# Kernel optimization log

Measured on AMD Instinct MI355X. Metric: run time of the kernel, lower is better.

The kernel has to match this reference:

```python
import jax, jax.numpy as jnp
import numpy as np
from functools import partial

VS, VT, E, H = 32000, 32000, 512, 1024
B, S, T = 32, 64, 64


def gru_cell(x, h, Wih, Whh, bih, bhh):
    # PyTorch GRU gate order: r, z, n
    gi = x @ Wih.T + bih
    gh = h @ Whh.T + bhh
    ir, iz, inn = jnp.split(gi, 3, axis=-1)
    hr, hz, hn = jnp.split(gh, 3, axis=-1)
    r = jax.nn.sigmoid(ir + hr)
    z = jax.nn.sigmoid(iz + hz)
    n = jnp.tanh(inn + r * hn)
    return (1.0 - z) * n + z * h


def setup_inputs() -> dict:
    key = jax.random.key(0)
    ks = jax.random.split(key, 20)
    s = 0.02
    src = jax.random.randint(ks[0], (B, S), 0, VS)
    tgt = jax.random.randint(ks[1], (B, T), 0, VT)
    src_embed = (jax.random.normal(ks[2], (VS, E)) * s).at[0].set(0.0)  # padding_idx=0
    tgt_embed = (jax.random.normal(ks[3], (VT, E)) * s).at[0].set(0.0)
    enc_Wih = jax.random.normal(ks[4], (3 * H, E)) * s
    enc_Whh = jax.random.normal(ks[5], (3 * H, H)) * s
    enc_bih = jax.random.normal(ks[6], (3 * H,)) * s
    enc_bhh = jax.random.normal(ks[7], (3 * H,)) * s
    dec_Wih = jax.random.normal(ks[8], (3 * H, E + H)) * s
    dec_Whh = jax.random.normal(ks[9], (3 * H, H)) * s
    dec_bih = jax.random.normal(ks[10], (3 * H,)) * s
    dec_bhh = jax.random.normal(ks[11], (3 * H,)) * s
    attn_W = jax.random.normal(ks[12], (E, 2 * H)) * s
    attn_b = jax.random.normal(ks[13], (E,)) * s
    v_w = jax.random.normal(ks[14], (E,)) * s
    fc_W = jax.random.normal(ks[15], (VT, H)) * s
    fc_b = jax.random.normal(ks[16], (VT,)) * s
    return dict(src=src, tgt=tgt, src_embed=src_embed, tgt_embed=tgt_embed,
                enc_Wih=enc_Wih, enc_Whh=enc_Whh, enc_bih=enc_bih, enc_bhh=enc_bhh,
                dec_Wih=dec_Wih, dec_Whh=dec_Whh, dec_bih=dec_bih, dec_bhh=dec_bhh,
                attn_W=attn_W, attn_b=attn_b, v_w=v_w, fc_W=fc_W, fc_b=fc_b)


def reference(src, tgt, src_embed, tgt_embed, enc_Wih, enc_Whh, enc_bih, enc_bhh,
              dec_Wih, dec_Whh, dec_bih, dec_bhh, attn_W, attn_b, v_w, fc_W, fc_b):
    # --- encoder: GRU over src ---
    src_emb = src_embed[src]                      # [B,S,E]
    h0 = jnp.zeros((src.shape[0], H), src_emb.dtype)

    def enc_step(h, x):
        h2 = gru_cell(x, h, enc_Wih, enc_Whh, enc_bih, enc_bhh)
        return h2, h2

    h_last, enc_seq = jax.lax.scan(enc_step, h0, jnp.swapaxes(src_emb, 0, 1))
    enc = jnp.swapaxes(enc_seq, 0, 1)             # [B,S,H] encoder_outputs

    # attn linear splits: cat([hidden, enc]) @ attn_W.T == h@Wh.T + enc@We.T
    Wh, We = attn_W[:, :H], attn_W[:, H:]
    enc_proj = jnp.einsum('bsh,eh->bse', enc, We) + attn_b  # [B,S,E]

    # --- decoder with teacher forcing ratio = 1.0 (deterministic) ---
    def dec_step(h, tok):
        emb = tgt_embed[tok]                              # [B,E]
        energy = jnp.tanh(enc_proj + (h @ Wh.T)[:, None, :])  # [B,S,E]
        scores = jnp.einsum('bse,e->bs', energy, v_w)
        w = jax.nn.softmax(scores, axis=1)                # [B,S]
        ctx = jnp.einsum('bs,bsh->bh', w, enc)            # [B,H]
        x = jnp.concatenate([emb, ctx], axis=-1)          # [B,E+H]
        h2 = gru_cell(x, h, dec_Wih, dec_Whh, dec_bih, dec_bhh)
        logits = h2 @ fc_W.T + fc_b                       # [B,VT]
        return h2, logits

    _, logits = jax.lax.scan(dec_step, h_last, tgt[:, :-1].T)  # [T-1,B,VT]
    return jnp.swapaxes(logits, 0, 1)                     # [B,T-1,VT]
```

## Files before the change

### kernel.cpp

```cpp
#include <hip/hip_runtime.h>
#include <hip/hip_bf16.h>

typedef __hip_bfloat16 bf16;
typedef __attribute__((ext_vector_type(8))) __bf16 bf16x8;
typedef __attribute__((ext_vector_type(4))) float f32x4;

#define DEVI __device__ __forceinline__

DEVI float sigm(float x) { return 1.f / (1.f + __expf(-x)); }
DEVI float tanh_fast(float x) { float e = __expf(2.f * x); return 1.f - 2.f / (e + 1.f); }
DEVI float us2f(unsigned short u) { return __uint_as_float(((unsigned)u) << 16); }

DEVI __bf16 f2b(float f) {
    unsigned u = __float_as_uint(f);
    u = u + 0x7FFFu + ((u >> 16) & 1u);
    unsigned short s = (unsigned short)(u >> 16);
    __bf16 b;
    __builtin_memcpy(&b, &s, 2);
    return b;
}

DEVI f32x4 MFMA(bf16x8 a, bf16x8 b, f32x4 c) {
    return __builtin_amdgcn_mfma_f32_16x16x32_bf16(a, b, c, 0, 0, 0);
}

DEVI bf16x8 load8(const bf16* p) { return *reinterpret_cast<const bf16x8*>(p); }
DEVI bf16x8 load8(const float* p) {
    float4 a = *reinterpret_cast<const float4*>(p);
    float4 b = *reinterpret_cast<const float4*>(p + 4);
    bf16x8 r;
    r[0] = f2b(a.x); r[1] = f2b(a.y); r[2] = f2b(a.z); r[3] = f2b(a.w);
    r[4] = f2b(b.x); r[5] = f2b(b.y); r[6] = f2b(b.z); r[7] = f2b(b.w);
    return r;
}

template<typename AT, typename BT, bool GATHER, bool SWAP>
__global__ __launch_bounds__(256)
void gemm_bt(const AT* __restrict__ A, const int* __restrict__ Aidx, int lda,
             const BT* __restrict__ B, int ldb, int boff,
             const float* __restrict__ bias,
             float* __restrict__ C, long ldc,
             int M_real, int K)
{
    __shared__ __attribute__((aligned(16))) bf16 As[128 * 32];
    __shared__ __attribute__((aligned(16))) bf16 Bs[128 * 32];
    const int tid = threadIdx.x;
    const int lane = tid & 63;
    const int w = tid >> 6;
    const int wr = w >> 1, wc = w & 1;
    const int bm = (SWAP ? blockIdx.x : blockIdx.y) * 128;
    const int bn = (SWAP ? blockIdx.y : blockIdx.x) * 128;

    const int l16_0 = (2 * w + 0) * 64 + lane;
    const int l16_1 = (2 * w + 1) * 64 + lane;
    const int row0 = l16_0 >> 2, c0 = l16_0 & 3;
    const int row1 = l16_1 >> 2, c1 = l16_1 & 3;

    long arow0 = GATHER ? (long)Aidx[bm + row0] : (long)(bm + row0);
    long arow1 = GATHER ? (long)Aidx[bm + row1] : (long)(bm + row1);
    const AT* agp0 = A + arow0 * lda + c0 * 8;
    const AT* agp1 = A + arow1 * lda + c1 * 8;
    const BT* bgp0 = B + (long)(bn + row0) * ldb + boff + c0 * 8;
    const BT* bgp1 = B + (long)(bn + row1) * ldb + boff + c1 * 8;

    f32x4 acc[4][4];
    #pragma unroll
    for (int i = 0; i < 4; i++)
        #pragma unroll
        for (int j = 0; j < 4; j++) acc[i][j] = f32x4{0.f, 0.f, 0.f, 0.f};

    const bf16x8* Asv = reinterpret_cast<const bf16x8*>(As);
    const bf16x8* Bsv = reinterpret_cast<const bf16x8*>(Bs);
    bf16x8* AsW = reinterpret_cast<bf16x8*>(As);
    bf16x8* BsW = reinterpret_cast<bf16x8*>(Bs);
    const int kq = lane >> 4;
    const int lrow = lane & 15;

    bf16x8 ra0 = load8(agp0);
    bf16x8 ra1 = load8(agp1);
    bf16x8 rb0 = load8(bgp0);
    bf16x8 rb1 = load8(bgp1);

    for (int k0 = 0; k0 < K; k0 += 32) {
        __syncthreads();
        AsW[l16_0] = ra0; AsW[l16_1] = ra1;
        BsW[l16_0] = rb0; BsW[l16_1] = rb1;
        __syncthreads();

        const int kn = k0 + 32;
        if (kn < K) {
            ra0 = load8(agp0 + kn);
            ra1 = load8(agp1 + kn);
            rb0 = load8(bgp0 + kn);
            rb1 = load8(bgp1 + kn);
        }

        bf16x8 af[4], bfr[4];
        #pragma unroll
        for (int mt = 0; mt < 4; mt++) af[mt] = Asv[(wr * 64 + mt * 16 + lrow) * 4 + kq];
        #pragma unroll
        for (int nt = 0; nt < 4; nt++) bfr[nt] = Bsv[(wc * 64 + nt * 16 + lrow) * 4 + kq];
        #pragma unroll
        for (int mt = 0; mt < 4; mt++)
            #pragma unroll
            for (int nt = 0; nt < 4; nt++)
                acc[mt][nt] = MFMA(af[mt], bfr[nt], acc[mt][nt]);
    }

    const int rbase = kq * 4;
    #pragma unroll
    for (int nt = 0; nt < 4; nt++) {
        const int col = bn + wc * 64 + nt * 16 + lrow;
        const float bv = bias[col];
        #pragma unroll
        for (int mt = 0; mt < 4; mt++) {
            const int rw = bm + wr * 64 + mt * 16 + rbase;
            #pragma unroll
            for (int r = 0; r < 4; r++) {
                const int row = rw + r;
                if (row < M_real) C[(long)row * ldc + col] = acc[mt][nt][r] + bv;
            }
        }
    }
}

__global__ __launch_bounds__(256)
void cvt_f32_bf16(const float* __restrict__ in, bf16* __restrict__ out, int n)
{
    int i = (blockIdx.x * blockDim.x + threadIdx.x) * 4;
    if (i < n) {
        float4 v = *reinterpret_cast<const float4*>(in + i);
        ushort4 o;
        __bf16 b0 = f2b(v.x), b1 = f2b(v.y), b2 = f2b(v.z), b3 = f2b(v.w);
        __builtin_memcpy(&o.x, &b0, 2); __builtin_memcpy(&o.y, &b1, 2);
        __builtin_memcpy(&o.z, &b2, 2); __builtin_memcpy(&o.w, &b3, 2);
        *reinterpret_cast<ushort4*>(out + i) = o;
    }
}

__global__ __launch_bounds__(512)
void enc_step(const bf16* __restrict__ h_bf, const float* __restrict__ h_f,
              const float* __restrict__ X, int t,
              const bf16* __restrict__ Whh, const float* __restrict__ bhh,
              float* __restrict__ h_f_n, bf16* __restrict__ h_bf_n,
              bf16* __restrict__ enc_out,
              const float* __restrict__ attnW, float* __restrict__ pa, int do_pa)
{
    __shared__ float part[8][3][32][16];
    __shared__ float h2s[32][16];
    const int tid = threadIdx.x;
    const int lane = tid & 63;
    const int kw = tid >> 6;
    const int j0 = blockIdx.x * 16;
    const int lrow = lane & 15;
    const int kq = lane >> 4;

    f32x4 acc[3][2];
    #pragma unroll
    for (int g = 0; g < 3; g++) { acc[g][0] = f32x4{0,0,0,0}; acc[g][1] = f32x4{0,0,0,0}; }

    const bf16x8* hv = reinterpret_cast<const bf16x8*>(h_bf);
    const bf16x8* wv = reinterpret_cast<const bf16x8*>(Whh);
    const int kb = kw * 16 + kq;
    const int a0r = lrow * 128 + kb;
    const int a1r = (16 + lrow) * 128 + kb;
    const int b0r = (j0 + lrow) * 128 + kb;
    const int b1r = (1024 + j0 + lrow) * 128 + kb;
    const int b2r = (2048 + j0 + lrow) * 128 + kb;

    #pragma unroll
    for (int kk = 0; kk < 4; kk++) {
        const int o = kk * 4;
        bf16x8 a0 = hv[a0r + o];
        bf16x8 a1 = hv[a1r + o];
        bf16x8 b0 = wv[b0r + o];
        bf16x8 b1 = wv[b1r + o];
        bf16x8 b2 = wv[b2r + o];
        acc[0][0] = MFMA(a0, b0, acc[0][0]); acc[0][1] = MFMA(a1, b0, acc[0][1]);
        acc[1][0] = MFMA(a0, b1, acc[1][0]); acc[1][1] = MFMA(a1, b1, acc[1][1]);
        acc[2][0] = MFMA(a0, b2, acc[2][0]); acc[2][1] = MFMA(a1, b2, acc[2][1]);
    }

    #pragma unroll
    for (int g = 0; g < 3; g++)
        #pragma unroll
        for (int mt = 0; mt < 2; mt++)
            #pragma unroll
            for (int r = 0; r < 4; r++)
                part[kw][g][mt * 16 + kq * 4 + r][lrow] = acc[g][mt][r];
    __syncthreads();

    const int b = tid >> 4, jc = tid & 15;
    const int j = j0 + jc;
    float s0 = 0.f, s1 = 0.f, s2 = 0.f;
    #pragma unroll
    for (int ww = 0; ww < 8; ww++) {
        s0 += part[ww][0][b][jc];
        s1 += part[ww][1][b][jc];
        s2 += part[ww][2][b][jc];
    }
    const size_t xi = ((size_t)b * 64 + t) * 3072 + j;
    float rr = sigm(X[xi] + s0 + bhh[j]);
    float zz = sigm(X[xi + 1024] + s1 + bhh[1024 + j]);
    float nn = tanh_fast(X[xi + 2048] + rr * (s2 + bhh[2048 + j]));
    float h2 = (1.f - zz) * nn + zz * h_f[b * 1024 + j];
    h_f_n[b * 1024 + j] = h2;
    bf16 hb = __float2bfloat16(h2);
    h_bf_n[b * 1024 + j] = hb;
    enc_out[((size_t)b * 64 + t) * 1024 + j] = hb;

    if (do_pa) {
        h2s[b][jc] = h2;
        __syncthreads();
        const int e = tid;
        const float* wr_ = attnW + (size_t)e * 2048 + j0;
        float wcol[16];
        #pragma unroll
        for (int k = 0; k < 16; k++) wcol[k] = wr_[k];
        float* po = pa + (size_t)blockIdx.x * 16384 + e;
        for (int bb = 0; bb < 32; bb++) {
            float s = 0.f;
            #pragma unroll
            for (int k = 0; k < 16; k++) s += wcol[k] * h2s[bb][k];
            po[bb * 512] = s;
        }
    }
}

__global__ __launch_bounds__(512)
void dec_step(const bf16* __restrict__ h_bf, const float* __restrict__ h_f,
              const bf16* __restrict__ ctx_bf,
              const float* __restrict__ X, int t,
              const bf16* __restrict__ Whh, const float* __restrict__ bhh,
              const bf16* __restrict__ Wih,
              float* __restrict__ h_f_n, bf16* __restrict__ h_bf_n,
              bf16* __restrict__ Hall,
              const float* __restrict__ attnW, float* __restrict__ pa, int do_pa)
{
    __shared__ float part[8][6][32][16];
    __shared__ float h2s[32][16];
    const int tid = threadIdx.x;
    const int lane = tid & 63;
    const int kw = tid >> 6;
    const int j0 = blockIdx.x * 16;
    const int lrow = lane & 15;
    const int kq = lane >> 4;

    f32x4 acc[6][2];
    #pragma unroll
    for (int g = 0; g < 6; g++) { acc[g][0] = f32x4{0,0,0,0}; acc[g][1] = f32x4{0,0,0,0}; }

    const bf16x8* hv = reinterpret_cast<const bf16x8*>(h_bf);
    const bf16x8* cv = reinterpret_cast<const bf16x8*>(ctx_bf);
    const bf16x8* wv = reinterpret_cast<const bf16x8*>(Whh);
    const bf16x8* uv = reinterpret_cast<const bf16x8*>(Wih);
    const int kb = kw * 16 + kq;
    const int hr0 = lrow * 128 + kb, hr1 = (16 + lrow) * 128 + kb;
    const int wb0 = (j0 + lrow) * 128 + kb;
    const int wb1 = (1024 + j0 + lrow) * 128 + kb;
    const int wb2 = (2048 + j0 + lrow) * 128 + kb;
    const int ub0 = (j0 + lrow) * 192 + 64 + kb;
    const int ub1 = (1024 + j0 + lrow) * 192 + 64 + kb;
    const int ub2 = (2048 + j0 + lrow) * 192 + 64 + kb;

    #pragma unroll
    for (int kk = 0; kk < 4; kk++) {
        const int o = kk * 4;
        bf16x8 ah0 = hv[hr0 + o], ah1 = hv[hr1 + o];
        bf16x8 ac0 = cv[hr0 + o], ac1 = cv[hr1 + o];
        bf16x8 b0 = wv[wb0 + o], b1 = wv[wb1 + o], b2 = wv[wb2 + o];
        bf16x8 u0 = uv[ub0 + o], u1 = uv[ub1 + o], u2 = uv[ub2 + o];
        acc[0][0] = MFMA(ah0, b0, acc[0][0]); acc[0][1] = MFMA(ah1, b0, acc[0][1]);
        acc[1][0] = MFMA(ah0, b1, acc[1][0]); acc[1][1] = MFMA(ah1, b1, acc[1][1]);
        acc[2][0] = MFMA(ah0, b2, acc[2][0]); acc[2][1] = MFMA(ah1, b2, acc[2][1]);
        acc[3][0] = MFMA(ac0, u0, acc[3][0]); acc[3][1] = MFMA(ac1, u0, acc[3][1]);
        acc[4][0] = MFMA(ac0, u1, acc[4][0]); acc[4][1] = MFMA(ac1, u1, acc[4][1]);
        acc[5][0] = MFMA(ac0, u2, acc[5][0]); acc[5][1] = MFMA(ac1, u2, acc[5][1]);
    }

    #pragma unroll
    for (int g = 0; g < 6; g++)
        #pragma unroll
        for (int mt = 0; mt < 2; mt++)
            #pragma unroll
            for (int r = 0; r < 4; r++)
                part[kw][g][mt * 16 + kq * 4 + r][lrow] = acc[g][mt][r];
    __syncthreads();

    const int b = tid >> 4, jc = tid & 15;
    const int j = j0 + jc;
    float h0 = 0.f, h1 = 0.f, h2g = 0.f, c0 = 0.f, c1 = 0.f, c2 = 0.f;
    #pragma unroll
    for (int ww = 0; ww < 8; ww++) {
        h0  += part[ww][0][b][jc];
        h1  += part[ww][1][b][jc];
        h2g += part[ww][2][b][jc];
        c0  += part[ww][3][b][jc];
        c1  += part[ww][4][b][jc];
        c2  += part[ww][5][b][jc];
    }
    const size_t xi = ((size_t)b * 63 + t) * 3072 + j;
    float rr = sigm(X[xi] + c0 + h0 + bhh[j]);
    float zz = sigm(X[xi + 1024] + c1 + h1 + bhh[1024 + j]);
    float nn = tanh_fast(X[xi + 2048] + c2 + rr * (h2g + bhh[2048 + j]));
    float h2 = (1.f - zz) * nn + zz * h_f[b * 1024 + j];
    h_f_n[b * 1024 + j] = h2;
    bf16 hb = __float2bfloat16(h2);
    h_bf_n[b * 1024 + j] = hb;
    Hall[((size_t)b * 63 + t) * 1024 + j] = hb;

    if (do_pa) {
        h2s[b][jc] = h2;
        __syncthreads();
        const int e = tid;
        const float* wr_ = attnW + (size_t)e * 2048 + j0;
        float wcol[16];
        #pragma unroll
        for (int k = 0; k < 16; k++) wcol[k] = wr_[k];
        float* po = pa + (size_t)blockIdx.x * 16384 + e;
        for (int bb = 0; bb < 32; bb++) {
            float s = 0.f;
            #pragma unroll
            for (int k = 0; k < 16; k++) s += wcol[k] * h2s[bb][k];
            po[bb * 512] = s;
        }
    }
}

__global__ __launch_bounds__(256)
void attn_step(const float* __restrict__ pa, const float* __restrict__ enc_pj,
               const bf16* __restrict__ enc, const float* __restrict__ v_w,
               bf16* __restrict__ ctx)
{
    __shared__ __attribute__((aligned(16))) float a_s[512];
    __shared__ __attribute__((aligned(16))) float vw_s[512];
    __shared__ float sc[64];
    __shared__ float wsm[64];
    const int b = blockIdx.x, tid = threadIdx.x;

    vw_s[tid] = v_w[tid];
    vw_s[256 + tid] = v_w[256 + tid];

    float sx = 0.f, sy = 0.f;
    const float* pb = pa + b * 512 + tid * 2;
    #pragma unroll 8
    for (int w = 0; w < 64; w++) {
        float2 v = *reinterpret_cast<const float2*>(pb + (size_t)w * 16384);
        sx += v.x; sy += v.y;
    }
    a_s[2 * tid] = sx; a_s[2 * tid + 1] = sy;
    __syncthreads();

    const int sI = tid >> 2, q = tid & 3;
    const float4* ep4 = reinterpret_cast<const float4*>(enc_pj + ((size_t)b * 64 + sI) * 512 + q * 128);
    const float4* as4 = reinterpret_cast<const float4*>(a_s + q * 128);
    const float4* vw4 = reinterpret_cast<const float4*>(vw_s + q * 128);
    float part = 0.f;
    #pragma unroll 4
    for (int e = 0; e < 32; e++) {
        float4 x = ep4[e], a = as4[e], v = vw4[e];
        part += v.x * tanh_fast(x.x + a.x);
        part += v.y * tanh_fast(x.y + a.y);
        part += v.z * tanh_fast(x.z + a.z);
        part += v.w * tanh_fast(x.w + a.w);
    }
    part += __shfl_xor(part, 1);
    part += __shfl_xor(part, 2);
    if (q == 0) sc[sI] = part;
    __syncthreads();

    if (tid < 64) {
        float v = sc[tid];
        float m = v;
        #pragma unroll
        for (int off = 32; off; off >>= 1) m = fmaxf(m, __shfl_xor(m, off));
        float e = __expf(v - m);
        float su = e;
        #pragma unroll
        for (int off = 32; off; off >>= 1) su += __shfl_xor(su, off);
        wsm[tid] = e / su;
    }
    __syncthreads();

    float c0 = 0, c1 = 0, c2 = 0, c3 = 0;
    const bf16* eb = enc + (size_t)b * 65536 + tid * 4;
    for (int s = 0; s < 64; s++) {
        float w = wsm[s];
        ushort4 u = *reinterpret_cast<const ushort4*>(eb + s * 1024);
        c0 += w * us2f(u.x); c1 += w * us2f(u.y);
        c2 += w * us2f(u.z); c3 += w * us2f(u.w);
    }
    ushort4 o;
    bf16 t0 = __float2bfloat16(c0), t1 = __float2bfloat16(c1);
    bf16 t2 = __float2bfloat16(c2), t3 = __float2bfloat16(c3);
    o.x = *(unsigned short*)&t0; o.y = *(unsigned short*)&t1;
    o.z = *(unsigned short*)&t2; o.w = *(unsigned short*)&t3;
    *reinterpret_cast<ushort4*>(ctx + b * 1024 + tid * 4) = o;
}

__global__ void init_k(float* __restrict__ h_f, bf16* __restrict__ h_bf,
                       bf16* __restrict__ hall_pad, int* __restrict__ idx_dec,
                       const int* __restrict__ tgt)
{
    const int i = blockIdx.x * blockDim.x + threadIdx.x;
    if (i < 32768) {
        h_f[i] = 0.f;
        h_bf[i] = __float2bfloat16(0.f);
        hall_pad[i] = __float2bfloat16(0.f);
    }
    if (i < 2048) {
        int v = 0;
        if (i < 2016) { int bb = i / 63; int tq = i - bb * 63; v = tgt[bb * 64 + tq]; }
        idx_dec[i] = v;
    }
}

extern "C" void kernel_launch(void* const* d_in, const int* in_sizes, int n_in,
                              void* d_out, int out_size, void* d_ws, size_t ws_size,
                              hipStream_t stream)
{
    const int*   src       = (const int*)d_in[0];
    const int*   tgt       = (const int*)d_in[1];
    const float* src_embed = (const float*)d_in[2];
    const float* tgt_embed = (const float*)d_in[3];
    const float* enc_Wih   = (const float*)d_in[4];
    const float* enc_Whh   = (const float*)d_in[5];
    const float* enc_bih   = (const float*)d_in[6];
    const float* enc_bhh   = (const float*)d_in[7];
    const float* dec_Wih   = (const float*)d_in[8];
    const float* dec_Whh   = (const float*)d_in[9];
    const float* dec_bih   = (const float*)d_in[10];
    const float* dec_bhh   = (const float*)d_in[11];
    const float* attn_W    = (const float*)d_in[12];
    const float* attn_b    = (const float*)d_in[13];
    const float* v_w       = (const float*)d_in[14];
    const float* fc_W      = (const float*)d_in[15];
    const float* fc_b      = (const float*)d_in[16];

    char* w = (char*)d_ws;
    float* X_enc      = (float*)(w);
    float* X_dec      = (float*)(w + 25165824);
    bf16*  enc_bf     = (bf16*) (w + 50331648);
    float* enc_pj     = (float*)(w + 54525952);
    bf16*  H_all      = (bf16*) (w + 58720256);
    float* h_f        = (float*)(w + 62914560);
    bf16*  h_bf       = (bf16*) (w + 63176704);
    bf16*  ctx_bf     = (bf16*) (w + 63307776);
    float* pa         = (float*)(w + 63373312);
    int*   idx_dec    = (int*)  (w + 67567616);
    bf16*  enc_Whh_bf = (bf16*) (w + 67575808);
    bf16*  dec_Whh_bf = (bf16*) (w + 73867264);
    bf16*  dec_Wih_bf = (bf16*) (w + 80158720);

    init_k<<<128, 256, 0, stream>>>(h_f, h_bf, H_all + 2016 * 1024, idx_dec, tgt);
    cvt_f32_bf16<<<3072, 256, 0, stream>>>(enc_Whh, enc_Whh_bf, 3145728);
    cvt_f32_bf16<<<3072, 256, 0, stream>>>(dec_Whh, dec_Whh_bf, 3145728);
    cvt_f32_bf16<<<4608, 256, 0, stream>>>(dec_Wih, dec_Wih_bf, 4718592);

    gemm_bt<float, float, true, false><<<dim3(24, 16), 256, 0, stream>>>(
        src_embed, src, 512, enc_Wih, 512, 0, enc_bih, X_enc, 3072, 2048, 512);
    gemm_bt<float, float, true, false><<<dim3(24, 16), 256, 0, stream>>>(
        tgt_embed, idx_dec, 512, dec_Wih, 1536, 0, dec_bih, X_dec, 3072, 2048, 512);

    for (int t = 0; t < 64; t++) {
        int cur = t & 1, nxt = cur ^ 1;
        enc_step<<<64, 512, 0, stream>>>(h_bf + cur * 32768, h_f + cur * 32768, X_enc, t,
                                         enc_Whh_bf, enc_bhh,
                                         h_f + nxt * 32768, h_bf + nxt * 32768, enc_bf,
                                         attn_W, pa, (t == 63) ? 1 : 0);
    }

    gemm_bt<bf16, float, false, false><<<dim3(4, 16), 256, 0, stream>>>(
        enc_bf, nullptr, 1024, attn_W, 2048, 1024, attn_b, enc_pj, 512, 2048, 1024);

    for (int t = 0; t < 63; t++) {
        int cur = t & 1, nxt = cur ^ 1;
        attn_step<<<32, 256, 0, stream>>>(pa, enc_pj, enc_bf, v_w, ctx_bf);
        dec_step<<<64, 512, 0, stream>>>(h_bf + cur * 32768, h_f + cur * 32768, ctx_bf,
                                         X_dec, t, dec_Whh_bf, dec_bhh, dec_Wih_bf,
                                         h_f + nxt * 32768, h_bf + nxt * 32768, H_all,
                                         attn_W, pa, (t < 62) ? 1 : 0);
    }

    gemm_bt<bf16, float, false, true><<<dim3(16, 250), 256, 0, stream>>>(
        H_all, nullptr, 1024, fc_W, 1024, 0, fc_b, (float*)d_out, 32000, 2016, 1024);
}
```

Baseline: 2.979 ms.

## Persistent grid-synced encoder/decoder loops and bf16 XCD-aware FC GEMM

Replaces the per-timestep encoder and decoder kernel launches with two persistent kernels that loop over time and use an atomic-counter grid barrier between steps. The attention step is folded into the decoder kernel, where 32 of the 64 blocks compute the context. The final vocabulary projection now pre-converts fc_W to bf16 and uses a new GEMM with a larger K tile and a block-index remap that groups tiles by XCD. This removes about 190 launch gaps and halves FC weight traffic. The cost is an extra conversion pass over fc_W and reliance on all 64 blocks being co-resident for the spin barrier.

```diff
diff --git a/kernel.cpp b/kernel.cpp
--- a/kernel.cpp
+++ b/kernel.cpp
@@ -19,6 +19,7 @@
     __builtin_memcpy(&b, &s, 2);
     return b;
 }
+DEVI unsigned short b2u(__bf16 b) { unsigned short s; __builtin_memcpy(&s, &b, 2); return s; }
 
 DEVI f32x4 MFMA(bf16x8 a, bf16x8 b, f32x4 c) {
     return __builtin_amdgcn_mfma_f32_16x16x32_bf16(a, b, c, 0, 0, 0);
@@ -34,7 +35,18 @@
     return r;
 }
 
-template<typename AT, typename BT, bool GATHER, bool SWAP>
+DEVI void grid_sync(unsigned* bar, unsigned target) {
+    __threadfence();
+    __syncthreads();
+    if (threadIdx.x == 0) {
+        atomicAdd(bar, 1u);
+        while (atomicAdd(bar, 0u) < target) __builtin_amdgcn_s_sleep(4);
+        __threadfence();
+    }
+    __syncthreads();
+}
+
+template<typename AT, typename BT, bool GATHER>
 __global__ __launch_bounds__(256)
 void gemm_bt(const AT* __restrict__ A, const int* __restrict__ Aidx, int lda,
              const BT* __restrict__ B, int ldb, int boff,
@@ -48,8 +60,8 @@
     const int lane = tid & 63;
     const int w = tid >> 6;
     const int wr = w >> 1, wc = w & 1;
-    const int bm = (SWAP ? blockIdx.x : blockIdx.y) * 128;
-    const int bn = (SWAP ? blockIdx.y : blockIdx.x) * 128;
+    const int bm = blockIdx.y * 128;
+    const int bn = blockIdx.x * 128;
 
     const int l16_0 = (2 * w + 0) * 64 + lane;
     const int l16_1 = (2 * w + 1) * 64 + lane;
@@ -125,26 +137,114 @@
 }
 
 __global__ __launch_bounds__(256)
+void gemm_fc(const bf16* __restrict__ A, const bf16* __restrict__ B,
+             const float* __restrict__ bias, float* __restrict__ C)
+{
+    __shared__ __attribute__((aligned(16))) bf16 As[8192];
+    __shared__ __attribute__((aligned(16))) bf16 Bs[8192];
+    const int tid = threadIdx.x;
+    const int bid = blockIdx.x;
+    const int xcd = bid & 7;
+    const int ii = bid >> 3;
+    const int p = xcd + 8 * (ii >> 4);
+    const int m = ii & 15;
+    if (p >= 250) return;
+    const int bm = m * 128, bn = p * 128;
+
+    const int lane = tid & 63, w = tid >> 6, wr = w >> 1, wc = w & 1;
+    const int kq = lane >> 4, lrow = lane & 15;
+
+    int rowc[4], c8c[4];
+    const bf16* gA[4];
+    const bf16* gB[4];
+    #pragma unroll
+    for (int c = 0; c < 4; c++) {
+        int q = c * 256 + tid;
+        rowc[c] = q >> 3; c8c[c] = q & 7;
+        gA[c] = A + (long)(bm + rowc[c]) * 1024 + c8c[c] * 8;
+        gB[c] = B + (long)(bn + rowc[c]) * 1024 + c8c[c] * 8;
+    }
+
+    f32x4 acc[4][4];
+    #pragma unroll
+    for (int i = 0; i < 4; i++)
+        #pragma unroll
+        for (int j = 0; j < 4; j++) acc[i][j] = f32x4{0.f, 0.f, 0.f, 0.f};
+
+    bf16x8* AsW = reinterpret_cast<bf16x8*>(As);
+    bf16x8* BsW = reinterpret_cast<bf16x8*>(Bs);
+    const bf16x8* Asv = reinterpret_cast<const bf16x8*>(As);
+    const bf16x8* Bsv = reinterpret_cast<const bf16x8*>(Bs);
+
+    bf16x8 ra[4], rb[4];
+    #pragma unroll
+    for (int c = 0; c < 4; c++) { ra[c] = load8(gA[c]); rb[c] = load8(gB[c]); }
+
+    for (int kt = 0; kt < 16; ++kt) {
+        __syncthreads();
+        #pragma unroll
+        for (int c = 0; c < 4; c++) {
+            AsW[c8c[c] * 128 + rowc[c]] = ra[c];
+            BsW[c8c[c] * 128 + rowc[c]] = rb[c];
+        }
+        __syncthreads();
+        if (kt < 15) {
+            const int ko = (kt + 1) * 64;
+            #pragma unroll
+            for (int c = 0; c < 4; c++) { ra[c] = load8(gA[c] + ko); rb[c] = load8(gB[c] + ko); }
+        }
+        #pragma unroll
+        for (int h = 0; h < 2; ++h) {
+            bf16x8 af[4], bfr[4];
+            #pragma unroll
+            for (int mt = 0; mt < 4; mt++) af[mt] = Asv[(h * 4 + kq) * 128 + wr * 64 + mt * 16 + lrow];
+            #pragma unroll
+            for (int nt = 0; nt < 4; nt++) bfr[nt] = Bsv[(h * 4 + kq) * 128 + wc * 64 + nt * 16 + lrow];
+            #pragma unroll
+            for (int mt = 0; mt < 4; mt++)
+                #pragma unroll
+                for (int nt = 0; nt < 4; nt++)
+                    acc[mt][nt] = MFMA(af[mt], bfr[nt], acc[mt][nt]);
+        }
+    }
+
+    const int rbase = kq * 4;
+    #pragma unroll
+    for (int nt = 0; nt < 4; nt++) {
+        const int col = bn + wc * 64 + nt * 16 + lrow;
+        const float bv = bias[col];
+        #pragma unroll
+        for (int mt = 0; mt < 4; mt++) {
+            const int rw = bm + wr * 64 + mt * 16 + rbase;
+            #pragma unroll
+            for (int r = 0; r < 4; r++) {
+                const int row = rw + r;
+                if (row < 2016) C[(long)row * 32000 + col] = acc[mt][nt][r] + bv;
+            }
+        }
+    }
+}
+
+__global__ __launch_bounds__(256)
 void cvt_f32_bf16(const float* __restrict__ in, bf16* __restrict__ out, int n)
 {
     int i = (blockIdx.x * blockDim.x + threadIdx.x) * 4;
     if (i < n) {
         float4 v = *reinterpret_cast<const float4*>(in + i);
         ushort4 o;
-        __bf16 b0 = f2b(v.x), b1 = f2b(v.y), b2 = f2b(v.z), b3 = f2b(v.w);
-        __builtin_memcpy(&o.x, &b0, 2); __builtin_memcpy(&o.y, &b1, 2);
-        __builtin_memcpy(&o.z, &b2, 2); __builtin_memcpy(&o.w, &b3, 2);
+        o.x = b2u(f2b(v.x)); o.y = b2u(f2b(v.y));
+        o.z = b2u(f2b(v.z)); o.w = b2u(f2b(v.w));
         *reinterpret_cast<ushort4*>(out + i) = o;
     }
 }
 
 __global__ __launch_bounds__(512)
-void enc_step(const bf16* __restrict__ h_bf, const float* __restrict__ h_f,
-              const float* __restrict__ X, int t,
-              const bf16* __restrict__ Whh, const float* __restrict__ bhh,
-              float* __restrict__ h_f_n, bf16* __restrict__ h_bf_n,
-              bf16* __restrict__ enc_out,
-              const float* __restrict__ attnW, float* __restrict__ pa, int do_pa)
+void enc_persist(bf16* __restrict__ h_bf, float* __restrict__ h_f,
+                 const float* __restrict__ X,
+                 const bf16* __restrict__ Whh, const float* __restrict__ bhh,
+                 bf16* __restrict__ enc_out,
+                 const float* __restrict__ attnW, float* __restrict__ pa,
+                 unsigned* __restrict__ bar)
 {
     __shared__ float part[8][3][32][16];
     __shared__ float h2s[32][16];
@@ -154,106 +254,110 @@
     const int j0 = blockIdx.x * 16;
     const int lrow = lane & 15;
     const int kq = lane >> 4;
-
-    f32x4 acc[3][2];
-    #pragma unroll
-    for (int g = 0; g < 3; g++) { acc[g][0] = f32x4{0,0,0,0}; acc[g][1] = f32x4{0,0,0,0}; }
-
-    const bf16x8* hv = reinterpret_cast<const bf16x8*>(h_bf);
-    const bf16x8* wv = reinterpret_cast<const bf16x8*>(Whh);
     const int kb = kw * 16 + kq;
     const int a0r = lrow * 128 + kb;
     const int a1r = (16 + lrow) * 128 + kb;
     const int b0r = (j0 + lrow) * 128 + kb;
     const int b1r = (1024 + j0 + lrow) * 128 + kb;
     const int b2r = (2048 + j0 + lrow) * 128 + kb;
-
-    #pragma unroll
-    for (int kk = 0; kk < 4; kk++) {
-        const int o = kk * 4;
-        bf16x8 a0 = hv[a0r + o];
-        bf16x8 a1 = hv[a1r + o];
-        bf16x8 b0 = wv[b0r + o];
-        bf16x8 b1 = wv[b1r + o];
-        bf16x8 b2 = wv[b2r + o];
-        acc[0][0] = MFMA(a0, b0, acc[0][0]); acc[0][1] = MFMA(a1, b0, acc[0][1]);
-        acc[1][0] = MFMA(a0, b1, acc[1][0]); acc[1][1] = MFMA(a1, b1, acc[1][1]);
-        acc[2][0] = MFMA(a0, b2, acc[2][0]); acc[2][1] = MFMA(a1, b2, acc[2][1]);
-    }
-
-    #pragma unroll
-    for (int g = 0; g < 3; g++)
-        #pragma unroll
-        for (int mt = 0; mt < 2; mt++)
-            #pragma unroll
-            for (int r = 0; r < 4; r++)
-                part[kw][g][mt * 16 + kq * 4 + r][lrow] = acc[g][mt][r];
-    __syncthreads();
-
-    const int b = tid >> 4, jc = tid & 15;
+    const bf16x8* wv = reinterpret_cast<const bf16x8*>(Whh);
+
+    const int bb = tid >> 4, jc = tid & 15;
     const int j = j0 + jc;
-    float s0 = 0.f, s1 = 0.f, s2 = 0.f;
-    #pragma unroll
-    for (int ww = 0; ww < 8; ww++) {
-        s0 += part[ww][0][b][jc];
-        s1 += part[ww][1][b][jc];
-        s2 += part[ww][2][b][jc];
-    }
-    const size_t xi = ((size_t)b * 64 + t) * 3072 + j;
-    float rr = sigm(X[xi] + s0 + bhh[j]);
-    float zz = sigm(X[xi + 1024] + s1 + bhh[1024 + j]);
-    float nn = tanh_fast(X[xi + 2048] + rr * (s2 + bhh[2048 + j]));
-    float h2 = (1.f - zz) * nn + zz * h_f[b * 1024 + j];
-    h_f_n[b * 1024 + j] = h2;
-    bf16 hb = __float2bfloat16(h2);
-    h_bf_n[b * 1024 + j] = hb;
-    enc_out[((size_t)b * 64 + t) * 1024 + j] = hb;
-
-    if (do_pa) {
-        h2s[b][jc] = h2;
+    const float bhr = bhh[j], bhz = bhh[1024 + j], bhn = bhh[2048 + j];
+    unsigned sn = 0;
+
+    for (int t = 0; t < 64; ++t) {
+        const int cur = t & 1;
+        const bf16x8* hv = reinterpret_cast<const bf16x8*>(h_bf) + cur * 4096;
+
+        f32x4 acc[3][2];
+        #pragma unroll
+        for (int g = 0; g < 3; g++) { acc[g][0] = f32x4{0,0,0,0}; acc[g][1] = f32x4{0,0,0,0}; }
+        #pragma unroll
+        for (int kk = 0; kk < 4; kk++) {
+            const int o = kk * 4;
+            bf16x8 a0 = hv[a0r + o];
+            bf16x8 a1 = hv[a1r + o];
+            bf16x8 b0 = wv[b0r + o];
+            bf16x8 b1 = wv[b1r + o];
+            bf16x8 b2 = wv[b2r + o];
+            acc[0][0] = MFMA(a0, b0, acc[0][0]); acc[0][1] = MFMA(a1, b0, acc[0][1]);
+            acc[1][0] = MFMA(a0, b1, acc[1][0]); acc[1][1] = MFMA(a1, b1, acc[1][1]);
+            acc[2][0] = MFMA(a0, b2, acc[2][0]); acc[2][1] = MFMA(a1, b2, acc[2][1]);
+        }
+        #pragma unroll
+        for (int g = 0; g < 3; g++)
+            #pragma unroll
+            for (int mt = 0; mt < 2; mt++)
+                #pragma unroll
+                for (int r = 0; r < 4; r++)
+                    part[kw][g][mt * 16 + kq * 4 + r][lrow] = acc[g][mt][r];
         __syncthreads();
-        const int e = tid;
-        const float* wr_ = attnW + (size_t)e * 2048 + j0;
-        float wcol[16];
-        #pragma unroll
-        for (int k = 0; k < 16; k++) wcol[k] = wr_[k];
-        float* po = pa + (size_t)blockIdx.x * 16384 + e;
-        for (int bb = 0; bb < 32; bb++) {
-            float s = 0.f;
-            #pragma unroll
-            for (int k = 0; k < 16; k++) s += wcol[k] * h2s[bb][k];
-            po[bb * 512] = s;
+
+        float s0 = 0.f, s1 = 0.f, s2 = 0.f;
+        #pragma unroll
+        for (int ww = 0; ww < 8; ww++) {
+            s0 += part[ww][0][bb][jc];
+            s1 += part[ww][1][bb][jc];
+            s2 += part[ww][2][bb][jc];
+        }
+        const size_t xi = ((size_t)bb * 64 + t) * 3072 + j;
+        float rr = sigm(X[xi] + s0 + bhr);
+        float zz = sigm(X[xi + 1024] + s1 + bhz);
+        float nn = tanh_fast(X[xi + 2048] + rr * (s2 + bhn));
+        float h2 = (1.f - zz) * nn + zz * h_f[cur * 32768 + bb * 1024 + j];
+        h_f[(cur ^ 1) * 32768 + bb * 1024 + j] = h2;
+        bf16 hb = __float2bfloat16(h2);
+        h_bf[(cur ^ 1) * 32768 + bb * 1024 + j] = hb;
+        enc_out[((size_t)bb * 64 + t) * 1024 + j] = hb;
+
+        if (t < 63) {
+            grid_sync(bar, ++sn * 64);
+        } else {
+            h2s[bb][jc] = h2;
+            __syncthreads();
+            const int e = tid;
+            const float* wr_ = attnW + (size_t)e * 2048 + j0;
+            float wcol[16];
+            #pragma unroll
+            for (int k = 0; k < 16; k++) wcol[k] = wr_[k];
+            float* po = pa + (size_t)blockIdx.x * 16384 + e;
+            for (int b2 = 0; b2 < 32; b2++) {
+                float s = 0.f;
+                #pragma unroll
+                for (int k = 0; k < 16; k++) s += wcol[k] * h2s[b2][k];
+                po[b2 * 512] = s;
+            }
         }
     }
 }
 
 __global__ __launch_bounds__(512)
-void dec_step(const bf16* __restrict__ h_bf, const float* __restrict__ h_f,
-              const bf16* __restrict__ ctx_bf,
-              const float* __restrict__ X, int t,
-              const bf16* __restrict__ Whh, const float* __restrict__ bhh,
-              const bf16* __restrict__ Wih,
-              float* __restrict__ h_f_n, bf16* __restrict__ h_bf_n,
-              bf16* __restrict__ Hall,
-              const float* __restrict__ attnW, float* __restrict__ pa, int do_pa)
+void dec_persist(bf16* __restrict__ h_bf, float* __restrict__ h_f,
+                 bf16* __restrict__ ctx_bf,
+                 const float* __restrict__ X,
+                 const bf16* __restrict__ Whh, const float* __restrict__ bhh,
+                 const bf16* __restrict__ Wih,
+                 bf16* __restrict__ Hall,
+                 const float* __restrict__ attnW, float* __restrict__ pa,
+                 const float* __restrict__ enc_pj, const bf16* __restrict__ enc,
+                 const float* __restrict__ v_w,
+                 unsigned* __restrict__ bar)
 {
     __shared__ float part[8][6][32][16];
     __shared__ float h2s[32][16];
+    __shared__ __attribute__((aligned(16))) float a_s[512];
+    __shared__ __attribute__((aligned(16))) float vw_s[512];
+    __shared__ float sc[64];
+    __shared__ float wsm[64];
+
     const int tid = threadIdx.x;
     const int lane = tid & 63;
     const int kw = tid >> 6;
     const int j0 = blockIdx.x * 16;
     const int lrow = lane & 15;
     const int kq = lane >> 4;
-
-    f32x4 acc[6][2];
-    #pragma unroll
-    for (int g = 0; g < 6; g++) { acc[g][0] = f32x4{0,0,0,0}; acc[g][1] = f32x4{0,0,0,0}; }
-
-    const bf16x8* hv = reinterpret_cast<const bf16x8*>(h_bf);
-    const bf16x8* cv = reinterpret_cast<const bf16x8*>(ctx_bf);
-    const bf16x8* wv = reinterpret_cast<const bf16x8*>(Whh);
-    const bf16x8* uv = reinterpret_cast<const bf16x8*>(Wih);
     const int kb = kw * 16 + kq;
     const int hr0 = lrow * 128 + kb, hr1 = (16 + lrow) * 128 + kb;
     const int wb0 = (j0 + lrow) * 128 + kb;
@@ -262,147 +366,148 @@
     const int ub0 = (j0 + lrow) * 192 + 64 + kb;
     const int ub1 = (1024 + j0 + lrow) * 192 + 64 + kb;
     const int ub2 = (2048 + j0 + lrow) * 192 + 64 + kb;
-
-    #pragma unroll
-    for (int kk = 0; kk < 4; kk++) {
-        const int o = kk * 4;
-        bf16x8 ah0 = hv[hr0 + o], ah1 = hv[hr1 + o];
-        bf16x8 ac0 = cv[hr0 + o], ac1 = cv[hr1 + o];
-        bf16x8 b0 = wv[wb0 + o], b1 = wv[wb1 + o], b2 = wv[wb2 + o];
-        bf16x8 u0 = uv[ub0 + o], u1 = uv[ub1 + o], u2 = uv[ub2 + o];
-        acc[0][0] = MFMA(ah0, b0, acc[0][0]); acc[0][1] = MFMA(ah1, b0, acc[0][1]);
-        acc[1][0] = MFMA(ah0, b1, acc[1][0]); acc[1][1] = MFMA(ah1, b1, acc[1][1]);
-        acc[2][0] = MFMA(ah0, b2, acc[2][0]); acc[2][1] = MFMA(ah1, b2, acc[2][1]);
-        acc[3][0] = MFMA(ac0, u0, acc[3][0]); acc[3][1] = MFMA(ac1, u0, acc[3][1]);
-        acc[4][0] = MFMA(ac0, u1, acc[4][0]); acc[4][1] = MFMA(ac1, u1, acc[4][1]);
-        acc[5][0] = MFMA(ac0, u2, acc[5][0]); acc[5][1] = MFMA(ac1, u2, acc[5][1]);
-    }
-
-    #pragma unroll
-    for (int g = 0; g < 6; g++)
-        #pragma unroll
-        for (int mt = 0; mt < 2; mt++)
-            #pragma unroll
-            for (int r = 0; r < 4; r++)
-                part[kw][g][mt * 16 + kq * 4 + r][lrow] = acc[g][mt][r];
+    const bf16x8* cv = reinterpret_cast<const bf16x8*>(ctx_bf);
+    const bf16x8* wv = reinterpret_cast<const bf16x8*>(Whh);
+    const bf16x8* uv = reinterpret_cast<const bf16x8*>(Wih);
+
+    const int bb = tid >> 4, jc = tid & 15;
+    const int j = j0 + jc;
+    const float bhr = bhh[j], bhz = bhh[1024 + j], bhn = bhh[2048 + j];
+
+    vw_s[tid] = v_w[tid];
     __syncthreads();
-
-    const int b = tid >> 4, jc = tid & 15;
-    const int j = j0 + jc;
-    float h0 = 0.f, h1 = 0.f, h2g = 0.f, c0 = 0.f, c1 = 0.f, c2 = 0.f;
-    #pragma unroll
-    for (int ww = 0; ww < 8; ww++) {
-        h0  += part[ww][0][b][jc];
-        h1  += part[ww][1][b][jc];
-        h2g += part[ww][2][b][jc];
-        c0  += part[ww][3][b][jc];
-        c1  += part[ww][4][b][jc];
-        c2  += part[ww][5][b][jc];
-    }
-    const size_t xi = ((size_t)b * 63 + t) * 3072 + j;
-    float rr = sigm(X[xi] + c0 + h0 + bhh[j]);
-    float zz = sigm(X[xi + 1024] + c1 + h1 + bhh[1024 + j]);
-    float nn = tanh_fast(X[xi + 2048] + c2 + rr * (h2g + bhh[2048 + j]));
-    float h2 = (1.f - zz) * nn + zz * h_f[b * 1024 + j];
-    h_f_n[b * 1024 + j] = h2;
-    bf16 hb = __float2bfloat16(h2);
-    h_bf_n[b * 1024 + j] = hb;
-    Hall[((size_t)b * 63 + t) * 1024 + j] = hb;
-
-    if (do_pa) {
-        h2s[b][jc] = h2;
+    unsigned sn = 0;
+
+    for (int t = 0; t < 63; ++t) {
+        const int cur = t & 1;
+
+        if (blockIdx.x < 32) {
+            const int b = blockIdx.x;
+            float s = 0.f;
+            const float* pb = pa + b * 512 + tid;
+            #pragma unroll 8
+            for (int wg = 0; wg < 64; wg++) s += pb[(size_t)wg * 16384];
+            a_s[tid] = s;
+            __syncthreads();
+
+            const int sI = tid >> 3, q = tid & 7;
+            const float4* ep4 = reinterpret_cast<const float4*>(enc_pj + ((size_t)b * 64 + sI) * 512 + q * 64);
+            const float4* as4 = reinterpret_cast<const float4*>(a_s + q * 64);
+            const float4* vw4 = reinterpret_cast<const float4*>(vw_s + q * 64);
+            float prt = 0.f;
+            #pragma unroll 4
+            for (int e = 0; e < 16; e++) {
+                float4 x = ep4[e], a = as4[e], v = vw4[e];
+                prt += v.x * tanh_fast(x.x + a.x);
+                prt += v.y * tanh_fast(x.y + a.y);
+                prt += v.z * tanh_fast(x.z + a.z);
+                prt += v.w * tanh_fast(x.w + a.w);
+            }
+            prt += __shfl_xor(prt, 1);
+            prt += __shfl_xor(prt, 2);
+            prt += __shfl_xor(prt, 4);
+            if (q == 0) sc[sI] = prt;
+            __syncthreads();
+
+            if (tid < 64) {
+                float v = sc[tid];
+                float mx = v;
+                #pragma unroll
+                for (int off = 32; off; off >>= 1) mx = fmaxf(mx, __shfl_xor(mx, off));
+                float e = __expf(v - mx);
+                float su = e;
+                #pragma unroll
+                for (int off = 32; off; off >>= 1) su += __shfl_xor(su, off);
+                wsm[tid] = e / su;
+            }
+            __syncthreads();
+
+            const int d0 = tid * 2;
+            float c0 = 0.f, c1 = 0.f;
+            const bf16* eb = enc + (size_t)b * 65536 + d0;
+            for (int s2 = 0; s2 < 64; s2++) {
+                float w = wsm[s2];
+                ushort2 u = *reinterpret_cast<const ushort2*>(eb + s2 * 1024);
+                c0 += w * us2f(u.x); c1 += w * us2f(u.y);
+            }
+            unsigned o = (unsigned)b2u(f2b(c0)) | ((unsigned)b2u(f2b(c1)) << 16);
+            *reinterpret_cast<unsigned*>(ctx_bf + b * 1024 + d0) = o;
+        }
+        grid_sync(bar, ++sn * 64);
+
+        const bf16x8* hv = reinterpret_cast<const bf16x8*>(h_bf) + cur * 4096;
+        f32x4 acc[6][2];
+        #pragma unroll
+        for (int g = 0; g < 6; g++) { acc[g][0] = f32x4{0,0,0,0}; acc[g][1] = f32x4{0,0,0,0}; }
+        #pragma unroll
+        for (int kk = 0; kk < 4; kk++) {
+            const int o = kk * 4;
+            bf16x8 ah0 = hv[hr0 + o], ah1 = hv[hr1 + o];
+            bf16x8 ac0 = cv[hr0 + o], ac1 = cv[hr1 + o];
+            bf16x8 b0 = wv[wb0 + o], b1 = wv[wb1 + o], b2 = wv[wb2 + o];
+            bf16x8 u0 = uv[ub0 + o], u1 = uv[ub1 + o], u2 = uv[ub2 + o];
+            acc[0][0] = MFMA(ah0, b0, acc[0][0]); acc[0][1] = MFMA(ah1, b0, acc[0][1]);
+            acc[1][0] = MFMA(ah0, b1, acc[1][0]); acc[1][1] = MFMA(ah1, b1, acc[1][1]);
+            acc[2][0] = MFMA(ah0, b2, acc[2][0]); acc[2][1] = MFMA(ah1, b2, acc[2][1]);
+            acc[3][0] = MFMA(ac0, u0, acc[3][0]); acc[3][1] = MFMA(ac1, u0, acc[3][1]);
+            acc[4][0] = MFMA(ac0, u1, acc[4][0]); acc[4][1] = MFMA(ac1, u1, acc[4][1]);
+            acc[5][0] = MFMA(ac0, u2, acc[5][0]); acc[5][1] = MFMA(ac1, u2, acc[5][1]);
+        }
+        #pragma unroll
+        for (int g = 0; g < 6; g++)
+            #pragma unroll
+            for (int mt = 0; mt < 2; mt++)
+                #pragma unroll
+                for (int r = 0; r < 4; r++)
+                    part[kw][g][mt * 16 + kq * 4 + r][lrow] = acc[g][mt][r];
         __syncthreads();
-        const int e = tid;
-        const float* wr_ = attnW + (size_t)e * 2048 + j0;
-        float wcol[16];
-        #pragma unroll
-        for (int k = 0; k < 16; k++) wcol[k] = wr_[k];
-        float* po = pa + (size_t)blockIdx.x * 16384 + e;
-        for (int bb = 0; bb < 32; bb++) {
-            float s = 0.f;
-            #pragma unroll
-            for (int k = 0; k < 16; k++) s += wcol[k] * h2s[bb][k];
-            po[bb * 512] = s;
-        }
-    }
-}
-
-__global__ __launch_bounds__(256)
-void attn_step(const float* __restrict__ pa, const float* __restrict__ enc_pj,
-               const bf16* __restrict__ enc, const float* __restrict__ v_w,
-               bf16* __restrict__ ctx)
-{
-    __shared__ __attribute__((aligned(16))) float a_s[512];
-    __shared__ __attribute__((aligned(16))) float vw_s[512];
-    __shared__ float sc[64];
-    __shared__ float wsm[64];
-    const int b = blockIdx.x, tid = threadIdx.x;
-
-    vw_s[tid] = v_w[tid];
-    vw_s[256 + tid] = v_w[256 + tid];
-
-    float sx = 0.f, sy = 0.f;
-    const float* pb = pa + b * 512 + tid * 2;
-    #pragma unroll 8
-    for (int w = 0; w < 64; w++) {
-        float2 v = *reinterpret_cast<const float2*>(pb + (size_t)w * 16384);
-        sx += v.x; sy += v.y;
-    }
-    a_s[2 * tid] = sx; a_s[2 * tid + 1] = sy;
-    __syncthreads();
-
-    const int sI = tid >> 2, q = tid & 3;
-    const float4* ep4 = reinterpret_cast<const float4*>(enc_pj + ((size_t)b * 64 + sI) * 512 + q * 128);
-    const float4* as4 = reinterpret_cast<const float4*>(a_s + q * 128);
-    const float4* vw4 = reinterpret_cast<const float4*>(vw_s + q * 128);
-    float part = 0.f;
-    #pragma unroll 4
-    for (int e = 0; e < 32; e++) {
-        float4 x = ep4[e], a = as4[e], v = vw4[e];
-        part += v.x * tanh_fast(x.x + a.x);
-        part += v.y * tanh_fast(x.y + a.y);
-        part += v.z * tanh_fast(x.z + a.z);
-        part += v.w * tanh_fast(x.w + a.w);
-    }
-    part += __shfl_xor(part, 1);
-    part += __shfl_xor(part, 2);
-    if (q == 0) sc[sI] = part;
-    __syncthreads();
-
-    if (tid < 64) {
-        float v = sc[tid];
-        float m = v;
-        #pragma unroll
-        for (int off = 32; off; off >>= 1) m = fmaxf(m, __shfl_xor(m, off));
-        float e = __expf(v - m);
-        float su = e;
-        #pragma unroll
-        for (int off = 32; off; off >>= 1) su += __shfl_xor(su, off);
-        wsm[tid] = e / su;
-    }
-    __syncthreads();
-
-    float c0 = 0, c1 = 0, c2 = 0, c3 = 0;
-    const bf16* eb = enc + (size_t)b * 65536 + tid * 4;
-    for (int s = 0; s < 64; s++) {
-        float w = wsm[s];
-        ushort4 u = *reinterpret_cast<const ushort4*>(eb + s * 1024);
-        c0 += w * us2f(u.x); c1 += w * us2f(u.y);
-        c2 += w * us2f(u.z); c3 += w * us2f(u.w);
-    }
-    ushort4 o;
-    bf16 t0 = __float2bfloat16(c0), t1 = __float2bfloat16(c1);
-    bf16 t2 = __float2bfloat16(c2), t3 = __float2bfloat16(c3);
-    o.x = *(unsigned short*)&t0; o.y = *(unsigned short*)&t1;
-    o.z = *(unsigned short*)&t2; o.w = *(unsigned short*)&t3;
-    *reinterpret_cast<ushort4*>(ctx + b * 1024 + tid * 4) = o;
+
+        float g0 = 0.f, g1 = 0.f, g2 = 0.f, c0 = 0.f, c1 = 0.f, c2 = 0.f;
+        #pragma unroll
+        for (int ww = 0; ww < 8; ww++) {
+            g0 += part[ww][0][bb][jc];
+            g1 += part[ww][1][bb][jc];
+            g2 += part[ww][2][bb][jc];
+            c0 += part[ww][3][bb][jc];
+            c1 += part[ww][4][bb][jc];
+            c2 += part[ww][5][bb][jc];
+        }
+        const size_t xi = ((size_t)bb * 63 + t) * 3072 + j;
+        float rr = sigm(X[xi] + c0 + g0 + bhr);
+        float zz = sigm(X[xi + 1024] + c1 + g1 + bhz);
+        float nn = tanh_fast(X[xi + 2048] + c2 + rr * (g2 + bhn));
+        float h2 = (1.f - zz) * nn + zz * h_f[cur * 32768 + bb * 1024 + j];
+        h_f[(cur ^ 1) * 32768 + bb * 1024 + j] = h2;
+        bf16 hb = __float2bfloat16(h2);
+        h_bf[(cur ^ 1) * 32768 + bb * 1024 + j] = hb;
+        Hall[((size_t)bb * 63 + t) * 1024 + j] = hb;
+
+        if (t < 62) {
+            h2s[bb][jc] = h2;
+            __syncthreads();
+            const int e = tid;
+            const float* wr_ = attnW + (size_t)e * 2048 + j0;
+            float wcol[16];
+            #pragma unroll
+            for (int k = 0; k < 16; k++) wcol[k] = wr_[k];
+            float* po = pa + (size_t)blockIdx.x * 16384 + e;
+            for (int b2 = 0; b2 < 32; b2++) {
+                float s = 0.f;
+                #pragma unroll
+                for (int k = 0; k < 16; k++) s += wcol[k] * h2s[b2][k];
+                po[b2 * 512] = s;
+            }
+            grid_sync(bar, ++sn * 64);
+        }
+    }
 }
 
 __global__ void init_k(float* __restrict__ h_f, bf16* __restrict__ h_bf,
                        bf16* __restrict__ hall_pad, int* __restrict__ idx_dec,
-                       const int* __restrict__ tgt)
+                       const int* __restrict__ tgt, unsigned* __restrict__ bar)
 {
     const int i = blockIdx.x * blockDim.x + threadIdx.x;
+    if (i < 64) bar[i] = 0u;
     if (i < 32768) {
         h_f[i] = 0.f;
         h_bf[i] = __float2bfloat16(0.f);
@@ -410,7 +515,7 @@
     }
     if (i < 2048) {
         int v = 0;
-        if (i < 2016) { int bb = i / 63; int tq = i - bb * 63; v = tgt[bb * 64 + tq]; }
+        if (i < 2016) { int b = i / 63; int tq = i - b * 63; v = tgt[b * 64 + tq]; }
         idx_dec[i] = v;
     }
 }
@@ -438,50 +543,43 @@
     const float* fc_b      = (const float*)d_in[16];
 
     char* w = (char*)d_ws;
-    float* X_enc      = (float*)(w);
-    float* X_dec      = (float*)(w + 25165824);
-    bf16*  enc_bf     = (bf16*) (w + 50331648);
-    float* enc_pj     = (float*)(w + 54525952);
-    bf16*  H_all      = (bf16*) (w + 58720256);
-    float* h_f        = (float*)(w + 62914560);
-    bf16*  h_bf       = (bf16*) (w + 63176704);
-    bf16*  ctx_bf     = (bf16*) (w + 63307776);
-    float* pa         = (float*)(w + 63373312);
-    int*   idx_dec    = (int*)  (w + 67567616);
-    bf16*  enc_Whh_bf = (bf16*) (w + 67575808);
-    bf16*  dec_Whh_bf = (bf16*) (w + 73867264);
-    bf16*  dec_Wih_bf = (bf16*) (w + 80158720);
-
-    init_k<<<128, 256, 0, stream>>>(h_f, h_bf, H_all + 2016 * 1024, idx_dec, tgt);
+    unsigned* bar       = (unsigned*)(w);
+    float* X_enc        = (float*)(w + 256);
+    float* X_dec        = (float*)(w + 25166080);
+    bf16*  enc_bf       = (bf16*) (w + 50331904);
+    float* enc_pj       = (float*)(w + 54526208);
+    bf16*  H_all        = (bf16*) (w + 58720512);
+    float* h_f          = (float*)(w + 62914816);
+    bf16*  h_bf         = (bf16*) (w + 63176960);
+    bf16*  ctx_bf       = (bf16*) (w + 63308032);
+    float* pa           = (float*)(w + 63373568);
+    int*   idx_dec      = (int*)  (w + 67567872);
+    bf16*  enc_Whh_bf   = (bf16*) (w + 67576064);
+    bf16*  dec_Whh_bf   = (bf16*) (w + 73867520);
+    bf16*  dec_Wih_bf   = (bf16*) (w + 80158976);
+    bf16*  fc_W_bf      = (bf16*) (w + 89596160);
+
+    init_k<<<128, 256, 0, stream>>>(h_f, h_bf, H_all + 2016 * 1024, idx_dec, tgt, bar);
     cvt_f32_bf16<<<3072, 256, 0, stream>>>(enc_Whh, enc_Whh_bf, 3145728);
     cvt_f32_bf16<<<3072, 256, 0, stream>>>(dec_Whh, dec_Whh_bf, 3145728);
     cvt_f32_bf16<<<4608, 256, 0, stream>>>(dec_Wih, dec_Wih_bf, 4718592);
-
-    gemm_bt<float, float, true, false><<<dim3(24, 16), 256, 0, stream>>>(
+    cvt_f32_bf16<<<32000, 256, 0, stream>>>(fc_W, fc_W_bf, 32768000);
+
+    gemm_bt<float, float, true><<<dim3(24, 16), 256, 0, stream>>>(
         src_embed, src, 512, enc_Wih, 512, 0, enc_bih, X_enc, 3072, 2048, 512);
-    gemm_bt<float, float, true, false><<<dim3(24, 16), 256, 0, stream>>>(
+    gemm_bt<float, float, true><<<dim3(24, 16), 256, 0, stream>>>(
         tgt_embed, idx_dec, 512, dec_Wih, 1536, 0, dec_bih, X_dec, 3072, 2048, 512);
 
-    for (int t = 0; t < 64; t++) {
-        int cur = t & 1, nxt = cur ^ 1;
-        enc_step<<<64, 512, 0, stream>>>(h_bf + cur * 32768, h_f + cur * 32768, X_enc, t,
-                                         enc_Whh_bf, enc_bhh,
-                                         h_f + nxt * 32768, h_bf + nxt * 32768, enc_bf,
-                                         attn_W, pa, (t == 63) ? 1 : 0);
-    }
-
-    gemm_bt<bf16, float, false, false><<<dim3(4, 16), 256, 0, stream>>>(
+    enc_persist<<<64, 512, 0, stream>>>(h_bf, h_f, X_enc, enc_Whh_bf, enc_bhh,
+                                        enc_bf, attn_W, pa, bar);
+
+    gemm_bt<bf16, float, false><<<dim3(4, 16), 256, 0, stream>>>(
         enc_bf, nullptr, 1024, attn_W, 2048, 1024, attn_b, enc_pj, 512, 2048, 1024);
 
-    for (int t = 0; t < 63; t++) {
-        int cur = t & 1, nxt = cur ^ 1;
-        attn_step<<<32, 256, 0, stream>>>(pa, enc_pj, enc_bf, v_w, ctx_bf);
-        dec_step<<<64, 512, 0, stream>>>(h_bf + cur * 32768, h_f + cur * 32768, ctx_bf,
-                                         X_dec, t, dec_Whh_bf, dec_bhh, dec_Wih_bf,
-                                         h_f + nxt * 32768, h_bf + nxt * 32768, H_all,
-                                         attn_W, pa, (t < 62) ? 1 : 0);
-    }
-
-    gemm_bt<bf16, float, false, true><<<dim3(16, 250), 256, 0, stream>>>(
-        H_all, nullptr, 1024, fc_W, 1024, 0, fc_b, (float*)d_out, 32000, 2016, 1024);
-}
+    dec_persist<<<64, 512, 0, stream>>>(h_bf, h_f, ctx_bf, X_dec,
+                                        dec_Whh_bf, dec_bhh, dec_Wih_bf,
+                                        H_all, attn_W, pa, enc_pj, enc_bf, v_w,
+                                        bar + 32);
+
+    gemm_fc<<<4096, 256, 0, stream>>>(H_all, fc_W_bf, fc_b, (float*)d_out);
+}
```

After: 7.563 ms. +153.9%, slower.
